# Kernel tuning notes

Measured on AMD Instinct MI355X. Metric: run time of the kernel, lower is better.

## Reference

```python
import jax, jax.numpy as jnp
import numpy as np

N, F_IN, H, C, E = 100000, 128, 128, 40, 600000


def setup_inputs() -> dict:
    key = jax.random.key(0)
    ks = jax.random.split(key, 20)
    s = 0.05
    inp = {
        "x": jax.random.normal(ks[0], (N, F_IN), jnp.float32),
        "edge_index": jax.random.randint(ks[1], (2, E), 0, N, jnp.int64),
        "importance": jnp.ones((F_IN,), jnp.float32),
        "W1": jax.random.normal(ks[2], (H, F_IN), jnp.float32) * s,
        "bl1": jax.random.normal(ks[3], (H,), jnp.float32) * s,
        "bc1": jnp.zeros((H,), jnp.float32),
        "W2": jax.random.normal(ks[4], (H, H), jnp.float32) * s,
        "bl2": jax.random.normal(ks[5], (H,), jnp.float32) * s,
        "bc2": jnp.zeros((H,), jnp.float32),
        "W3": jax.random.normal(ks[6], (H, H), jnp.float32) * s,
        "bl3": jax.random.normal(ks[7], (H,), jnp.float32) * s,
        "bc3": jnp.zeros((H,), jnp.float32),
        "Wlin1": jax.random.normal(ks[8], (H, H), jnp.float32) * s,
        "blin1": jax.random.normal(ks[9], (H,), jnp.float32) * s,
        "Wlin2": jax.random.normal(ks[10], (C, H), jnp.float32) * s,
        "blin2": jax.random.normal(ks[11], (C,), jnp.float32) * s,
    }
    return inp


def balanced_conv(x, W, bl, bc, row, col):
    # lin, then symmetric-normalized message, mean-aggregated over targets
    n = x.shape[0]
    h = x @ W.T + bl                                   # [N, H]
    loops = jnp.arange(n)
    r = jnp.concatenate([row, loops])                  # sources (x_j index)
    c = jnp.concatenate([col, loops])                  # targets
    deg = jnp.zeros((n,), x.dtype).at[c].add(1.0)      # degree(col) incl. self-loops
    dinv = deg ** -0.5
    norm = dinv[r] * dinv[c]                           # [E+N]
    msg = norm[:, None] * h[r]                         # gather + scale
    agg = jnp.zeros((n, h.shape[1]), x.dtype).at[c].add(msg)  # scatter-add
    return agg / deg[:, None] + bc                     # mean aggr + bias


def reference(x, edge_index, importance, W1, bl1, bc1, W2, bl2, bc2,
              W3, bl3, bc3, Wlin1, blin1, Wlin2, blin2):
    row, col = edge_index[0], edge_index[1]
    h = x * importance
    h = jax.nn.relu(balanced_conv(h, W1, bl1, bc1, row, col))
    h = jax.nn.relu(balanced_conv(h, W2, bl2, bc2, row, col))
    h = jax.nn.relu(balanced_conv(h, W3, bl3, bc3, row, col))
    h = jax.nn.relu(h @ Wlin1.T + blin1)
    h = h @ Wlin2.T + blin2
    return jax.nn.log_softmax(h, axis=-1)
```

## Files before the change

### kernel.cpp

```cpp
#include <hip/hip_runtime.h>
#include <hip/hip_bf16.h>

#define F 128
#define C_CLS 40
#define NWSPLIT 35
#define ELLCAP 32

typedef __attribute__((ext_vector_type(8))) short short8;
typedef __attribute__((ext_vector_type(4))) float float4v;
typedef unsigned short ushort;

__device__ inline float bf2f(ushort u) {
  unsigned int x = ((unsigned int)u) << 16;
  return __builtin_bit_cast(float, x);
}
__device__ inline ushort f2bf(float f) {
  __hip_bfloat16 h = __float2bfloat16(f);
  return __builtin_bit_cast(ushort, h);
}
__device__ inline void split_bf16(float f, ushort& hi, ushort& lo) {
  hi = f2bf(f);
  lo = f2bf(f - bf2f(hi));
}
__device__ inline int swz(int lane) { return lane ^ ((lane >> 4) & 3); }

__global__ __launch_bounds__(256) void setup_kernel(
    const float* __restrict__ W1, const float* __restrict__ imp,
    const float* __restrict__ W2, const float* __restrict__ W3,
    const float* __restrict__ Wl1, const float* __restrict__ Wh2,
    const float* __restrict__ x,
    ushort* __restrict__ WhP,
    ushort* __restrict__ W2hH, ushort* __restrict__ W2lH,
    const int* __restrict__ row, const int* __restrict__ col,
    int* __restrict__ cnt, int* __restrict__ ell, ushort* __restrict__ X16,
    int ne, int n, int nbE) {
  int b = blockIdx.x;
  if (b < NWSPLIT) {
    int ci = b * 256 + threadIdx.x;
    if (ci < 8192) {
      const float* src[4] = {W1, W2, W3, Wl1};
      int p = ci >> 11, c = ci & 2047;
      int kc = c >> 10, ct = (c >> 7) & 7, ks = (c >> 6) & 1, ln = c & 63;
      int dl = swz(ln);
      int colw = ct * 16 + (dl & 15);
      int k = kc * 64 + ks * 32 + (dl >> 4) * 8;
      float4 f0 = *(const float4*)&src[p][(size_t)colw * F + k];
      float4 f1 = *(const float4*)&src[p][(size_t)colw * F + k + 4];
      float v[8] = {f0.x, f0.y, f0.z, f0.w, f1.x, f1.y, f1.z, f1.w};
      if (p == 0) {
        float4 i0 = *(const float4*)&imp[k];
        float4 i1 = *(const float4*)&imp[k + 4];
        v[0] *= i0.x; v[1] *= i0.y; v[2] *= i0.z; v[3] *= i0.w;
        v[4] *= i1.x; v[5] *= i1.y; v[6] *= i1.z; v[7] *= i1.w;
      }
      ushort hi[8];
#pragma unroll
      for (int j = 0; j < 8; ++j) hi[j] = f2bf(v[j]);
      *(short8*)&WhP[(size_t)ci * 8] = *(short8*)hi;
    } else if (ci < 8192 + 768) {
      int c = ci - 8192;
      int ct = c >> 8, ks = (c >> 6) & 3, ln = c & 63;
      int colw = ct * 16 + (ln & 15);
      int k = ks * 32 + (ln >> 4) * 8;
      float v[8];
      if (colw < C_CLS) {
        float4 f0 = *(const float4*)&Wh2[(size_t)colw * F + k];
        float4 f1 = *(const float4*)&Wh2[(size_t)colw * F + k + 4];
        v[0] = f0.x; v[1] = f0.y; v[2] = f0.z; v[3] = f0.w;
        v[4] = f1.x; v[5] = f1.y; v[6] = f1.z; v[7] = f1.w;
      } else {
#pragma unroll
        for (int j = 0; j < 8; ++j) v[j] = 0.f;
      }
      ushort hi[8], lo[8];
#pragma unroll
      for (int j = 0; j < 8; ++j) split_bf16(v[j], hi[j], lo[j]);
      *(short8*)&W2hH[(size_t)c * 8] = *(short8*)hi;
      *(short8*)&W2lH[(size_t)c * 8] = *(short8*)lo;
    }
  } else if (b < NWSPLIT + nbE) {
    int e = (b - NWSPLIT) * 256 + threadIdx.x;
    if (e < ne) {
      int r = row[e], c = col[e];
      int p = atomicAdd(&cnt[c], 1);
      if (p < ELLCAP) ell[(size_t)c * ELLCAP + p] = r;
    }
  } else {
    int i = (b - NWSPLIT - nbE) * 2048 + threadIdx.x * 8;
    if (i < n * F) {
      float4 f0 = *(const float4*)&x[i];
      float4 f1 = *(const float4*)&x[i + 4];
      ushort o[8] = {f2bf(f0.x), f2bf(f0.y), f2bf(f0.z), f2bf(f0.w),
                     f2bf(f1.x), f2bf(f1.y), f2bf(f1.z), f2bf(f1.w)};
      *(short8*)&X16[i] = *(short8*)o;
    }
  }
}

__global__ __launch_bounds__(256, 2) void conv_fused(
    const int* __restrict__ cnt, const int* __restrict__ ell,
    const ushort* __restrict__ Xin, const ushort* __restrict__ Wh,
    const float* __restrict__ bl, const float* __restrict__ bc,
    ushort* __restrict__ OUT, int n) {
  __shared__ ushort sWh[16384];
  const int t = threadIdx.x;
#pragma unroll
  for (int pp = 0; pp < 8; ++pp) {
    int ci = t + pp * 256;
    *(short8*)&sWh[ci * 8] = *(const short8*)&Wh[(size_t)ci * 8];
  }
  const int w = t >> 6, lane = t & 63, quad = lane >> 4, cl = lane & 15;
  const int node = blockIdx.x * 64 + w * 16 + cl;

  float acc[4][8];
#pragma unroll
  for (int ks = 0; ks < 4; ++ks)
#pragma unroll
    for (int q = 0; q < 8; ++q) acc[ks][q] = 0.f;

  float gsum = 0.f, dc = 0.f, id = 0.f;
  int lim = 0;
  if (node < n) {
    int cv = cnt[node];
    float d = (float)(cv + 1);
    dc = rsqrtf(d);
    id = 1.0f / d;
    lim = cv < ELLCAP ? cv : ELLCAP;
  }
  const int4* ep = (const int4*)&ell[(size_t)node * ELLCAP];
  const int qoff = quad * 8;

  for (int base = 0; base < lim; base += 4) {
    int4 rr = ep[base >> 2];
    bool p1 = base + 1 < lim, p2 = base + 2 < lim, p3 = base + 3 < lim;
    int r1 = p1 ? rr.y : rr.x;
    int r2 = p2 ? rr.z : rr.x;
    int r3 = p3 ? rr.w : rr.x;
    float g0 = rsqrtf((float)(cnt[rr.x] + 1));
    float g1 = p1 ? rsqrtf((float)(cnt[r1] + 1)) : 0.f;
    float g2 = p2 ? rsqrtf((float)(cnt[r2] + 1)) : 0.f;
    float g3 = p3 ? rsqrtf((float)(cnt[r3] + 1)) : 0.f;
    gsum += (g0 + g1) + (g2 + g3);
    const ushort* q0 = &Xin[(size_t)rr.x * F + qoff];
    const ushort* q1 = &Xin[(size_t)r1 * F + qoff];
    const ushort* q2 = &Xin[(size_t)r2 * F + qoff];
    const ushort* q3 = &Xin[(size_t)r3 * F + qoff];
#pragma unroll
    for (int ks = 0; ks < 4; ++ks) {
      short8 v0 = *(const short8*)&q0[ks * 32];
      short8 v1 = *(const short8*)&q1[ks * 32];
      short8 v2 = *(const short8*)&q2[ks * 32];
      short8 v3 = *(const short8*)&q3[ks * 32];
#pragma unroll
      for (int q = 0; q < 8; ++q) {
        float t0 = g0 * bf2f((ushort)v0[q]) + g1 * bf2f((ushort)v1[q]);
        float t1 = g2 * bf2f((ushort)v2[q]) + g3 * bf2f((ushort)v3[q]);
        acc[ks][q] += t0 + t1;
      }
    }
  }

  short8 sfrag[4];
  float wsum = dc * gsum + id;
  if (node < n) {
    const ushort* sq = &Xin[(size_t)node * F + qoff];
#pragma unroll
    for (int ks = 0; ks < 4; ++ks) {
      short8 sv = *(const short8*)&sq[ks * 32];
      ushort o[8];
#pragma unroll
      for (int q = 0; q < 8; ++q)
        o[q] = f2bf(dc * acc[ks][q] + id * bf2f((ushort)sv[q]));
      sfrag[ks] = *(short8*)o;
    }
  } else {
#pragma unroll
    for (int ks = 0; ks < 4; ++ks) sfrag[ks] = (short8){0, 0, 0, 0, 0, 0, 0, 0};
  }
  __syncthreads();

  float4v co[8];
#pragma unroll
  for (int mt = 0; mt < 8; ++mt) co[mt] = (float4v){0.f, 0.f, 0.f, 0.f};
  const int sl = swz(lane);
#pragma unroll
  for (int ks = 0; ks < 4; ++ks) {
    const int base2 = ((ks >> 1) * 1024 + (ks & 1) * 64 + sl) * 8;
#pragma unroll
    for (int mt = 0; mt < 8; ++mt) {
      short8 a_h = *(short8*)&sWh[base2 + mt * 128 * 8];
      co[mt] = __builtin_amdgcn_mfma_f32_16x16x32_bf16(a_h, sfrag[ks], co[mt], 0, 0, 0);
    }
  }

  if (node < n) {
#pragma unroll
    for (int mt = 0; mt < 8; ++mt) {
      float4 blv = *(const float4*)&bl[mt * 16 + quad * 4];
      float4 bcv = *(const float4*)&bc[mt * 16 + quad * 4];
      ushort o[4];
      o[0] = f2bf(fmaxf((co[mt][0] + wsum * blv.x) * id + bcv.x, 0.f));
      o[1] = f2bf(fmaxf((co[mt][1] + wsum * blv.y) * id + bcv.y, 0.f));
      o[2] = f2bf(fmaxf((co[mt][2] + wsum * blv.z) * id + bcv.z, 0.f));
      o[3] = f2bf(fmaxf((co[mt][3] + wsum * blv.w) * id + bcv.w, 0.f));
      *(ushort4*)&OUT[(size_t)node * F + mt * 16 + quad * 4] = *(ushort4*)o;
    }
  }
}

__global__ __launch_bounds__(256, 2) void head_fused(const ushort* __restrict__ X,
    const ushort* __restrict__ Wl1h, const float* __restrict__ bl,
    const ushort* __restrict__ W2h, const ushort* __restrict__ W2l,
    const float* __restrict__ b2, float* __restrict__ out, int nrows) {
  __shared__ ushort sWh[16384];
  __shared__ ushort sW2h[6144], sW2l[6144];
  __shared__ ushort sH[8192];
  __shared__ float b2s[48];
  const int t = threadIdx.x;
#pragma unroll
  for (int pp = 0; pp < 8; ++pp) {
    int ci = t + pp * 256;
    *(short8*)&sWh[ci * 8] = *(const short8*)&Wl1h[(size_t)ci * 8];
  }
#pragma unroll
  for (int pp = 0; pp < 3; ++pp) {
    int c = t + pp * 256;
    *(short8*)&sW2h[c * 8] = *(const short8*)&W2h[(size_t)c * 8];
    *(short8*)&sW2l[c * 8] = *(const short8*)&W2l[(size_t)c * 8];
  }
  if (t < 48) b2s[t] = (t < C_CLS) ? b2[t] : -1e30f;
  __syncthreads();

  const int w = t >> 6, lane = t & 63;
  const int quad = lane >> 4, cl = lane & 15;
  const int sl = swz(lane);
  const int row0 = (blockIdx.x * 4 + w) * 16;
  char* sHb = (char*)sH;

  float4v acc1[8];
#pragma unroll
  for (int mt = 0; mt < 8; ++mt) acc1[mt] = (float4v){0.f, 0.f, 0.f, 0.f};
  const int gr1 = row0 + cl;
#pragma unroll
  for (int ks = 0; ks < 4; ++ks) {
    short8 b;
    if (gr1 < nrows) b = *(const short8*)&X[(size_t)gr1 * F + ks * 32 + quad * 8];
    else b = (short8){0, 0, 0, 0, 0, 0, 0, 0};
    const int base = ((ks >> 1) * 1024 + (ks & 1) * 64 + sl) * 8;
#pragma unroll
    for (int mt = 0; mt < 8; ++mt) {
      short8 a_h = *(short8*)&sWh[base + mt * 128 * 8];
      acc1[mt] = __builtin_amdgcn_mfma_f32_16x16x32_bf16(a_h, b, acc1[mt], 0, 0, 0);
    }
  }
#pragma unroll
  for (int mt = 0; mt < 8; ++mt) {
    float4 bv = *(const float4*)&bl[mt * 16 + quad * 4];
    ushort o[4];
    o[0] = f2bf(fmaxf(acc1[mt][0] + bv.x, 0.f));
    o[1] = f2bf(fmaxf(acc1[mt][1] + bv.y, 0.f));
    o[2] = f2bf(fmaxf(acc1[mt][2] + bv.z, 0.f));
    o[3] = f2bf(fmaxf(acc1[mt][3] + bv.w, 0.f));
    int ch = (mt * 2 + (quad >> 1)) ^ cl;
    *(ushort4*)&sHb[w * 4096 + cl * 256 + ch * 16 + (quad & 1) * 8] = *(ushort4*)o;
  }
  __syncthreads();

  float4v acc[3];
#pragma unroll
  for (int ct = 0; ct < 3; ++ct) acc[ct] = (float4v){0.f, 0.f, 0.f, 0.f};
#pragma unroll
  for (int ks = 0; ks < 4; ++ks) {
    int ch2 = (ks * 4 + quad) ^ cl;
    short8 a = *(short8*)&sHb[w * 4096 + cl * 256 + ch2 * 16];
#pragma unroll
    for (int ct = 0; ct < 3; ++ct) {
      int chunk = ((ct * 4 + ks) * 64 + lane) * 8;
      short8 b_h = *(short8*)&sW2h[chunk];
      short8 b_l = *(short8*)&sW2l[chunk];
      acc[ct] = __builtin_amdgcn_mfma_f32_16x16x32_bf16(a, b_h, acc[ct], 0, 0, 0);
      acc[ct] = __builtin_amdgcn_mfma_f32_16x16x32_bf16(a, b_l, acc[ct], 0, 0, 0);
    }
  }

  float b0 = b2s[cl], b1 = b2s[16 + cl], b2v = b2s[32 + cl];
  float lse[4];
#pragma unroll
  for (int reg = 0; reg < 4; ++reg) {
    float v0 = acc[0][reg] + b0;
    float v1 = acc[1][reg] + b1;
    float v2 = acc[2][reg] + b2v;
    acc[0][reg] = v0; acc[1][reg] = v1; acc[2][reg] = v2;
    float m = fmaxf(fmaxf(v0, v1), v2);
#pragma unroll
    for (int o = 1; o < 16; o <<= 1) m = fmaxf(m, __shfl_xor(m, o));
    float s = __expf(v0 - m) + __expf(v1 - m) + __expf(v2 - m);
#pragma unroll
    for (int o = 1; o < 16; o <<= 1) s += __shfl_xor(s, o);
    lse[reg] = logf(s) + m;
  }
#pragma unroll
  for (int reg = 0; reg < 4; ++reg) {
    int gr = row0 + quad * 4 + reg;
    if (gr < nrows) {
      out[(size_t)gr * C_CLS + cl] = acc[0][reg] - lse[reg];
      out[(size_t)gr * C_CLS + 16 + cl] = acc[1][reg] - lse[reg];
      if (cl < 8) out[(size_t)gr * C_CLS + 32 + cl] = acc[2][reg] - lse[reg];
    }
  }
}

extern "C" void kernel_launch(void* const* d_in, const int* in_sizes, int n_in,
                              void* d_out, int out_size, void* d_ws, size_t ws_size,
                              hipStream_t stream) {
  const float* x    = (const float*)d_in[0];
  const int*   ei   = (const int*)d_in[1];
  const float* imp  = (const float*)d_in[2];
  const float* W1   = (const float*)d_in[3];
  const float* bl1  = (const float*)d_in[4];
  const float* bc1  = (const float*)d_in[5];
  const float* W2   = (const float*)d_in[6];
  const float* bl2  = (const float*)d_in[7];
  const float* bc2  = (const float*)d_in[8];
  const float* W3   = (const float*)d_in[9];
  const float* bl3  = (const float*)d_in[10];
  const float* bc3  = (const float*)d_in[11];
  const float* Wl1  = (const float*)d_in[12];
  const float* bli1 = (const float*)d_in[13];
  const float* Wl2  = (const float*)d_in[14];
  const float* bli2 = (const float*)d_in[15];
  float* out = (float*)d_out;

  const int N = in_sizes[0] / F;
  const int E = in_sizes[1] / 2;

  ushort* A16 = (ushort*)d_ws;
  ushort* B16 = A16 + (size_t)N * F;
  ushort* WhP = B16 + (size_t)N * F;
  ushort* W2hH = WhP + 65536;
  ushort* W2lH = W2hH + 6144;
  int*   cnt  = (int*)(W2lH + 6144);
  int*   ell  = cnt + N;

  const int* rowv = ei;
  const int* colv = ei + E;

  int nbE  = (E + 255) / 256;
  int nbX  = (N * F + 2047) / 2048;
  int nbCv = (N + 63) / 64;
  int nbHd = (N + 63) / 64;

  hipMemsetAsync(cnt, 0, (size_t)N * sizeof(int), stream);
  setup_kernel<<<NWSPLIT + nbE + nbX, 256, 0, stream>>>(
      W1, imp, W2, W3, Wl1, Wl2, x, WhP, W2hH, W2lH, rowv, colv, cnt, ell, B16,
      E, N, nbE);

  conv_fused<<<nbCv, 256, 0, stream>>>(cnt, ell, B16, WhP,         bl1, bc1, A16, N);
  conv_fused<<<nbCv, 256, 0, stream>>>(cnt, ell, A16, WhP + 16384, bl2, bc2, B16, N);
  conv_fused<<<nbCv, 256, 0, stream>>>(cnt, ell, B16, WhP + 32768, bl3, bc3, A16, N);

  head_fused<<<nbHd, 256, 0, stream>>>(A16, WhP + 49152, bli1, W2hH, W2lH, bli2, out, N);
}
```

Before: 329.3 us.

## Pre-scale features by dinv, precompute weight sums, pad ELL with zero row

```diff
diff --git a/kernel.cpp b/kernel.cpp
--- a/kernel.cpp
+++ b/kernel.cpp
@@ -28,12 +28,11 @@
     const float* __restrict__ W1, const float* __restrict__ imp,
     const float* __restrict__ W2, const float* __restrict__ W3,
     const float* __restrict__ Wl1, const float* __restrict__ Wh2,
-    const float* __restrict__ x,
     ushort* __restrict__ WhP,
     ushort* __restrict__ W2hH, ushort* __restrict__ W2lH,
     const int* __restrict__ row, const int* __restrict__ col,
-    int* __restrict__ cnt, int* __restrict__ ell, ushort* __restrict__ X16,
-    int ne, int n, int nbE) {
+    int* __restrict__ cnt, int* __restrict__ ell,
+    int ne, int n) {
   int b = blockIdx.x;
   if (b < NWSPLIT) {
     int ci = b * 256 + threadIdx.x;
@@ -78,37 +77,71 @@
       *(short8*)&W2hH[(size_t)c * 8] = *(short8*)hi;
       *(short8*)&W2lH[(size_t)c * 8] = *(short8*)lo;
     }
-  } else if (b < NWSPLIT + nbE) {
+  } else {
     int e = (b - NWSPLIT) * 256 + threadIdx.x;
     if (e < ne) {
       int r = row[e], c = col[e];
       int p = atomicAdd(&cnt[c], 1);
       if (p < ELLCAP) ell[(size_t)c * ELLCAP + p] = r;
     }
-  } else {
-    int i = (b - NWSPLIT - nbE) * 2048 + threadIdx.x * 8;
-    if (i < n * F) {
+  }
+}
+
+__global__ __launch_bounds__(256) void prepass_kernel(
+    const float* __restrict__ x, const int* __restrict__ cnt,
+    int* __restrict__ ell, float* __restrict__ wsum,
+    ushort* __restrict__ Xs, ushort* __restrict__ Az,
+    int n, int nbW, int nbX) {
+  int b = blockIdx.x;
+  if (b < nbW) {
+    int node = b * 256 + threadIdx.x;
+    if (node >= n) return;
+    int cv = cnt[node];
+    int lim = cv < ELLCAP ? cv : ELLCAP;
+    int lim4 = (lim + 3) & ~3;
+    float gs = 0.f;
+    const int4* ep = (const int4*)&ell[(size_t)node * ELLCAP];
+    for (int base = 0; base < lim; base += 4) {
+      int4 rr = ep[base >> 2];
+      bool p1 = base + 1 < lim, p2 = base + 2 < lim, p3 = base + 3 < lim;
+      int r1 = p1 ? rr.y : rr.x;
+      int r2 = p2 ? rr.z : rr.x;
+      int r3 = p3 ? rr.w : rr.x;
+      float g0 = rsqrtf((float)(cnt[rr.x] + 1));
+      float g1 = p1 ? rsqrtf((float)(cnt[r1] + 1)) : 0.f;
+      float g2 = p2 ? rsqrtf((float)(cnt[r2] + 1)) : 0.f;
+      float g3 = p3 ? rsqrtf((float)(cnt[r3] + 1)) : 0.f;
+      gs += (g0 + g1) + (g2 + g3);
+    }
+    float d = (float)(cv + 1);
+    wsum[node] = rsqrtf(d) * gs + 1.0f / d;
+    for (int p = lim; p < lim4; ++p) ell[(size_t)node * ELLCAP + p] = n;
+  } else if (b < nbW + nbX) {
+    size_t i = (size_t)(b - nbW) * 2048 + (size_t)threadIdx.x * 8;
+    if (i < (size_t)n * F) {
+      int node = (int)(i >> 7);
+      float dc = rsqrtf((float)(cnt[node] + 1));
       float4 f0 = *(const float4*)&x[i];
       float4 f1 = *(const float4*)&x[i + 4];
-      ushort o[8] = {f2bf(f0.x), f2bf(f0.y), f2bf(f0.z), f2bf(f0.w),
-                     f2bf(f1.x), f2bf(f1.y), f2bf(f1.z), f2bf(f1.w)};
-      *(short8*)&X16[i] = *(short8*)o;
-    }
-  }
-}
-
-__global__ __launch_bounds__(256, 2) void conv_fused(
+      ushort o[8] = {f2bf(dc * f0.x), f2bf(dc * f0.y), f2bf(dc * f0.z), f2bf(dc * f0.w),
+                     f2bf(dc * f1.x), f2bf(dc * f1.y), f2bf(dc * f1.z), f2bf(dc * f1.w)};
+      *(short8*)&Xs[i] = *(short8*)o;
+    }
+  } else {
+    int t = threadIdx.x;
+    short8 z = (short8){0, 0, 0, 0, 0, 0, 0, 0};
+    if (t < 16) *(short8*)&Xs[(size_t)n * F + t * 8] = z;
+    else if (t < 32) *(short8*)&Az[(size_t)n * F + (t - 16) * 8] = z;
+  }
+}
+
+template <bool SCALE_OUT>
+__global__ __launch_bounds__(256) void conv_fused(
     const int* __restrict__ cnt, const int* __restrict__ ell,
-    const ushort* __restrict__ Xin, const ushort* __restrict__ Wh,
-    const float* __restrict__ bl, const float* __restrict__ bc,
-    ushort* __restrict__ OUT, int n) {
-  __shared__ ushort sWh[16384];
+    const ushort* __restrict__ Xs, const ushort* __restrict__ Wh,
+    const float* __restrict__ wsum, const float* __restrict__ bl,
+    const float* __restrict__ bc, ushort* __restrict__ OUT, int n) {
   const int t = threadIdx.x;
-#pragma unroll
-  for (int pp = 0; pp < 8; ++pp) {
-    int ci = t + pp * 256;
-    *(short8*)&sWh[ci * 8] = *(const short8*)&Wh[(size_t)ci * 8];
-  }
   const int w = t >> 6, lane = t & 63, quad = lane >> 4, cl = lane & 15;
   const int node = blockIdx.x * 64 + w * 16 + cl;
 
@@ -118,33 +151,25 @@
 #pragma unroll
     for (int q = 0; q < 8; ++q) acc[ks][q] = 0.f;
 
-  float gsum = 0.f, dc = 0.f, id = 0.f;
-  int lim = 0;
+  float dc = 1.f, id = 1.f;
+  int lim4 = 0;
   if (node < n) {
     int cv = cnt[node];
     float d = (float)(cv + 1);
     dc = rsqrtf(d);
     id = 1.0f / d;
-    lim = cv < ELLCAP ? cv : ELLCAP;
+    int lim = cv < ELLCAP ? cv : ELLCAP;
+    lim4 = (lim + 3) & ~3;
   }
   const int4* ep = (const int4*)&ell[(size_t)node * ELLCAP];
   const int qoff = quad * 8;
 
-  for (int base = 0; base < lim; base += 4) {
+  for (int base = 0; base < lim4; base += 4) {
     int4 rr = ep[base >> 2];
-    bool p1 = base + 1 < lim, p2 = base + 2 < lim, p3 = base + 3 < lim;
-    int r1 = p1 ? rr.y : rr.x;
-    int r2 = p2 ? rr.z : rr.x;
-    int r3 = p3 ? rr.w : rr.x;
-    float g0 = rsqrtf((float)(cnt[rr.x] + 1));
-    float g1 = p1 ? rsqrtf((float)(cnt[r1] + 1)) : 0.f;
-    float g2 = p2 ? rsqrtf((float)(cnt[r2] + 1)) : 0.f;
-    float g3 = p3 ? rsqrtf((float)(cnt[r3] + 1)) : 0.f;
-    gsum += (g0 + g1) + (g2 + g3);
-    const ushort* q0 = &Xin[(size_t)rr.x * F + qoff];
-    const ushort* q1 = &Xin[(size_t)r1 * F + qoff];
-    const ushort* q2 = &Xin[(size_t)r2 * F + qoff];
-    const ushort* q3 = &Xin[(size_t)r3 * F + qoff];
+    const ushort* q0 = &Xs[(size_t)rr.x * F + qoff];
+    const ushort* q1 = &Xs[(size_t)rr.y * F + qoff];
+    const ushort* q2 = &Xs[(size_t)rr.z * F + qoff];
+    const ushort* q3 = &Xs[(size_t)rr.w * F + qoff];
 #pragma unroll
     for (int ks = 0; ks < 4; ++ks) {
       short8 v0 = *(const short8*)&q0[ks * 32];
@@ -153,31 +178,29 @@
       short8 v3 = *(const short8*)&q3[ks * 32];
 #pragma unroll
       for (int q = 0; q < 8; ++q) {
-        float t0 = g0 * bf2f((ushort)v0[q]) + g1 * bf2f((ushort)v1[q]);
-        float t1 = g2 * bf2f((ushort)v2[q]) + g3 * bf2f((ushort)v3[q]);
+        float t0 = bf2f((ushort)v0[q]) + bf2f((ushort)v1[q]);
+        float t1 = bf2f((ushort)v2[q]) + bf2f((ushort)v3[q]);
         acc[ks][q] += t0 + t1;
       }
     }
   }
 
   short8 sfrag[4];
-  float wsum = dc * gsum + id;
   if (node < n) {
-    const ushort* sq = &Xin[(size_t)node * F + qoff];
+    const ushort* sq = &Xs[(size_t)node * F + qoff];
 #pragma unroll
     for (int ks = 0; ks < 4; ++ks) {
       short8 sv = *(const short8*)&sq[ks * 32];
       ushort o[8];
 #pragma unroll
       for (int q = 0; q < 8; ++q)
-        o[q] = f2bf(dc * acc[ks][q] + id * bf2f((ushort)sv[q]));
+        o[q] = f2bf(dc * (acc[ks][q] + bf2f((ushort)sv[q])));
       sfrag[ks] = *(short8*)o;
     }
   } else {
 #pragma unroll
     for (int ks = 0; ks < 4; ++ks) sfrag[ks] = (short8){0, 0, 0, 0, 0, 0, 0, 0};
   }
-  __syncthreads();
 
   float4v co[8];
 #pragma unroll
@@ -188,48 +211,36 @@
     const int base2 = ((ks >> 1) * 1024 + (ks & 1) * 64 + sl) * 8;
 #pragma unroll
     for (int mt = 0; mt < 8; ++mt) {
-      short8 a_h = *(short8*)&sWh[base2 + mt * 128 * 8];
+      short8 a_h = *(const short8*)&Wh[base2 + mt * 1024];
       co[mt] = __builtin_amdgcn_mfma_f32_16x16x32_bf16(a_h, sfrag[ks], co[mt], 0, 0, 0);
     }
   }
 
   if (node < n) {
+    float ws = wsum[node];
 #pragma unroll
     for (int mt = 0; mt < 8; ++mt) {
       float4 blv = *(const float4*)&bl[mt * 16 + quad * 4];
       float4 bcv = *(const float4*)&bc[mt * 16 + quad * 4];
-      ushort o[4];
-      o[0] = f2bf(fmaxf((co[mt][0] + wsum * blv.x) * id + bcv.x, 0.f));
-      o[1] = f2bf(fmaxf((co[mt][1] + wsum * blv.y) * id + bcv.y, 0.f));
-      o[2] = f2bf(fmaxf((co[mt][2] + wsum * blv.z) * id + bcv.z, 0.f));
-      o[3] = f2bf(fmaxf((co[mt][3] + wsum * blv.w) * id + bcv.w, 0.f));
+      float v0 = fmaxf((co[mt][0] + ws * blv.x) * id + bcv.x, 0.f);
+      float v1 = fmaxf((co[mt][1] + ws * blv.y) * id + bcv.y, 0.f);
+      float v2 = fmaxf((co[mt][2] + ws * blv.z) * id + bcv.z, 0.f);
+      float v3 = fmaxf((co[mt][3] + ws * blv.w) * id + bcv.w, 0.f);
+      if (SCALE_OUT) { v0 *= dc; v1 *= dc; v2 *= dc; v3 *= dc; }
+      ushort o[4] = {f2bf(v0), f2bf(v1), f2bf(v2), f2bf(v3)};
       *(ushort4*)&OUT[(size_t)node * F + mt * 16 + quad * 4] = *(ushort4*)o;
     }
   }
 }
 
-__global__ __launch_bounds__(256, 2) void head_fused(const ushort* __restrict__ X,
+__global__ __launch_bounds__(256) void head_fused(const ushort* __restrict__ X,
     const ushort* __restrict__ Wl1h, const float* __restrict__ bl,
     const ushort* __restrict__ W2h, const ushort* __restrict__ W2l,
     const float* __restrict__ b2, float* __restrict__ out, int nrows) {
-  __shared__ ushort sWh[16384];
-  __shared__ ushort sW2h[6144], sW2l[6144];
   __shared__ ushort sH[8192];
   __shared__ float b2s[48];
   const int t = threadIdx.x;
-#pragma unroll
-  for (int pp = 0; pp < 8; ++pp) {
-    int ci = t + pp * 256;
-    *(short8*)&sWh[ci * 8] = *(const short8*)&Wl1h[(size_t)ci * 8];
-  }
-#pragma unroll
-  for (int pp = 0; pp < 3; ++pp) {
-    int c = t + pp * 256;
-    *(short8*)&sW2h[c * 8] = *(const short8*)&W2h[(size_t)c * 8];
-    *(short8*)&sW2l[c * 8] = *(const short8*)&W2l[(size_t)c * 8];
-  }
   if (t < 48) b2s[t] = (t < C_CLS) ? b2[t] : -1e30f;
-  __syncthreads();
 
   const int w = t >> 6, lane = t & 63;
   const int quad = lane >> 4, cl = lane & 15;
@@ -249,7 +260,7 @@
     const int base = ((ks >> 1) * 1024 + (ks & 1) * 64 + sl) * 8;
 #pragma unroll
     for (int mt = 0; mt < 8; ++mt) {
-      short8 a_h = *(short8*)&sWh[base + mt * 128 * 8];
+      short8 a_h = *(const short8*)&Wl1h[base + mt * 1024];
       acc1[mt] = __builtin_amdgcn_mfma_f32_16x16x32_bf16(a_h, b, acc1[mt], 0, 0, 0);
     }
   }
@@ -276,8 +287,8 @@
 #pragma unroll
     for (int ct = 0; ct < 3; ++ct) {
       int chunk = ((ct * 4 + ks) * 64 + lane) * 8;
-      short8 b_h = *(short8*)&sW2h[chunk];
-      short8 b_l = *(short8*)&sW2l[chunk];
+      short8 b_h = *(const short8*)&W2h[chunk];
+      short8 b_l = *(const short8*)&W2l[chunk];
       acc[ct] = __builtin_amdgcn_mfma_f32_16x16x32_bf16(a, b_h, acc[ct], 0, 0, 0);
       acc[ct] = __builtin_amdgcn_mfma_f32_16x16x32_bf16(a, b_l, acc[ct], 0, 0, 0);
     }
@@ -335,29 +346,32 @@
   const int E = in_sizes[1] / 2;
 
   ushort* A16 = (ushort*)d_ws;
-  ushort* B16 = A16 + (size_t)N * F;
-  ushort* WhP = B16 + (size_t)N * F;
+  ushort* B16 = A16 + (size_t)(N + 1) * F;
+  ushort* WhP = B16 + (size_t)(N + 1) * F;
   ushort* W2hH = WhP + 65536;
   ushort* W2lH = W2hH + 6144;
-  int*   cnt  = (int*)(W2lH + 6144);
+  float* wsum = (float*)(W2lH + 6144);
+  int*   cnt  = (int*)(wsum + N);
   int*   ell  = cnt + N;
 
   const int* rowv = ei;
   const int* colv = ei + E;
 
   int nbE  = (E + 255) / 256;
+  int nbW  = (N + 255) / 256;
   int nbX  = (N * F + 2047) / 2048;
   int nbCv = (N + 63) / 64;
   int nbHd = (N + 63) / 64;
 
   hipMemsetAsync(cnt, 0, (size_t)N * sizeof(int), stream);
-  setup_kernel<<<NWSPLIT + nbE + nbX, 256, 0, stream>>>(
-      W1, imp, W2, W3, Wl1, Wl2, x, WhP, W2hH, W2lH, rowv, colv, cnt, ell, B16,
-      E, N, nbE);
-
-  conv_fused<<<nbCv, 256, 0, stream>>>(cnt, ell, B16, WhP,         bl1, bc1, A16, N);
-  conv_fused<<<nbCv, 256, 0, stream>>>(cnt, ell, A16, WhP + 16384, bl2, bc2, B16, N);
-  conv_fused<<<nbCv, 256, 0, stream>>>(cnt, ell, B16, WhP + 32768, bl3, bc3, A16, N);
+  setup_kernel<<<NWSPLIT + nbE, 256, 0, stream>>>(
+      W1, imp, W2, W3, Wl1, Wl2, WhP, W2hH, W2lH, rowv, colv, cnt, ell, E, N);
+  prepass_kernel<<<nbW + nbX + 1, 256, 0, stream>>>(
+      x, cnt, ell, wsum, B16, A16, N, nbW, nbX);
+
+  conv_fused<true ><<<nbCv, 256, 0, stream>>>(cnt, ell, B16, WhP,         wsum, bl1, bc1, A16, N);
+  conv_fused<true ><<<nbCv, 256, 0, stream>>>(cnt, ell, A16, WhP + 16384, wsum, bl2, bc2, B16, N);
+  conv_fused<false><<<nbCv, 256, 0, stream>>>(cnt, ell, B16, WhP + 32768, wsum, bl3, bc3, A16, N);
 
   head_fused<<<nbHd, 256, 0, stream>>>(A16, WhP + 49152, bli1, W2hH, W2lH, bli2, out, N);
 }
```

New measurement: 347.3 us. +5.5%, slower.
